# Kernel tuning notes

Hardware: AMD Instinct MI355X
Metric: run time of the kernel (lower is better)

The kernel has to match this reference:

```python
import jax, jax.numpy as jnp
import numpy as np

B, S, D, H, L = 2, 2048, 768, 12, 12
DH = D // H
REL_POS_BINS, MAX_REL_POS = 32, 128
REL_2D_POS_BINS, MAX_REL_2D_POS = 64, 256
LN_EPS = 1e-12


def setup_inputs() -> dict:
    key = jax.random.key(0)
    ks = jax.random.split(key, 12)
    s = 0.02
    return {
        "hidden_states": jax.random.normal(ks[0], (B, S, D), jnp.float32),
        "attention_mask": jnp.zeros((B, 1, 1, S), jnp.bool_),  # True = masked
        "position_ids": jnp.sort(jax.random.randint(ks[1], (B, S), 0, 1024), axis=-1),
        "bbox": jax.random.randint(ks[2], (B, S, 4), 0, 1024),
        # stacked per-layer params (torch Linear applied as x @ W + b)
        "q_w": jax.random.normal(ks[3], (L, D, D), jnp.float32) * s,
        "q_b": jnp.zeros((L, D), jnp.float32),
        "k_w": jax.random.normal(ks[4], (L, D, D), jnp.float32) * s,
        "k_b": jnp.zeros((L, D), jnp.float32),
        "v_w": jax.random.normal(ks[5], (L, D, D), jnp.float32) * s,
        "v_b": jnp.zeros((L, D), jnp.float32),
        "o_w": jax.random.normal(ks[6], (L, D, D), jnp.float32) * s,
        "o_b": jnp.zeros((L, D), jnp.float32),
        "ln_g": jnp.ones((L, D), jnp.float32),
        "ln_b": jnp.zeros((L, D), jnp.float32),
        # rel-pos bias heads x buckets (nn.Linear(bins, heads, bias=False).weight)
        "rel_pos_bias_w": jax.random.normal(ks[7], (H, REL_POS_BINS), jnp.float32) * s,
        "rel_x_bias_w": jax.random.normal(ks[8], (H, REL_2D_POS_BINS), jnp.float32) * s,
        "rel_y_bias_w": jax.random.normal(ks[9], (H, REL_2D_POS_BINS), jnp.float32) * s,
    }


def _rel_bucket(rel, num_buckets, max_distance):
    # bidirectional bucketing from Mesh-TF / ErnieLayout
    nb = num_buckets // 2
    ret = (rel > 0).astype(jnp.int32) * nb
    n = jnp.abs(rel).astype(jnp.int32)
    max_exact = nb // 2
    is_small = n < max_exact
    nf = jnp.maximum(n, 1).astype(jnp.float32)  # avoid log(0); masked by is_small
    val_large = max_exact + (
        jnp.log(nf / max_exact) / np.log(max_distance / max_exact) * (nb - max_exact)
    ).astype(jnp.int32)
    val_large = jnp.minimum(val_large, nb - 1)
    return ret + jnp.where(is_small, n, val_large)


def _bias_from_table(ids_1d, table, num_buckets, max_distance):
    # ids_1d: [B,S] int; table: [H, buckets] -> bias [B,H,S,S]
    rel = ids_1d[:, None, :] - ids_1d[:, :, None]  # memory - query
    buckets = _rel_bucket(rel, num_buckets, max_distance)  # [B,S,S]
    return jnp.transpose(table.T[buckets], (0, 3, 1, 2))  # one-hot @ W.T == gather


def _layer_norm(x, g, b):
    m = jnp.mean(x, axis=-1, keepdims=True)
    v = jnp.mean((x - m) ** 2, axis=-1, keepdims=True)
    return (x - m) / jnp.sqrt(v + LN_EPS) * g + b


def reference(hidden_states, attention_mask, position_ids, bbox,
              q_w, q_b, k_w, k_b, v_w, v_b, o_w, o_b, ln_g, ln_b,
              rel_pos_bias_w, rel_x_bias_w, rel_y_bias_w):
    rel_pos = _bias_from_table(position_ids, rel_pos_bias_w, REL_POS_BINS, MAX_REL_POS)
    rel_2d = (_bias_from_table(bbox[:, :, 0], rel_x_bias_w, REL_2D_POS_BINS, MAX_REL_2D_POS)
              + _bias_from_table(bbox[:, :, 3], rel_y_bias_w, REL_2D_POS_BINS, MAX_REL_2D_POS))
    bias = rel_pos + rel_2d  # [B,H,S,S], shared across layers
    neg = jnp.finfo(jnp.float32).min
    inv_sqrt_dh = 1.0 / np.sqrt(DH)

    def layer(h, p):
        qw, qb, kw, kb, vw, vb, ow, ob, g, bb = p
        q = (h @ qw + qb).reshape(B, S, H, DH).transpose(0, 2, 1, 3) * inv_sqrt_dh
        k = (h @ kw + kb).reshape(B, S, H, DH).transpose(0, 2, 1, 3)
        v = (h @ vw + vb).reshape(B, S, H, DH).transpose(0, 2, 1, 3)
        scores = jnp.einsum('bhqd,bhkd->bhqk', q, k) + bias
        scores = jnp.where(attention_mask, neg, scores)
        probs = jax.nn.softmax(scores, axis=-1)
        ctx = jnp.einsum('bhqk,bhkd->bhqd', probs, v).transpose(0, 2, 1, 3).reshape(B, S, D)
        out = ctx @ ow + ob  # ErnieLayoutSelfOutput dense
        return _layer_norm(out + h, g, bb), None

    h, _ = jax.lax.scan(layer, hidden_states,
                        (q_w, q_b, k_w, k_b, v_w, v_b, o_w, o_b, ln_g, ln_b))
    return h
```

## Files before the change

### kernel.cpp

```cpp
#include <hip/hip_runtime.h>


#define BB 2
#define SS 2048
#define DD 768
#define HH 12
#define NLAYER 12
#define MM 4096

typedef unsigned short u16;
typedef __attribute__((ext_vector_type(8))) short bf16x8;
typedef __attribute__((ext_vector_type(4))) float f32x4;

#define LOG2E 1.44269504088896340736f

__device__ __forceinline__ u16 f2bf(float f) {
  unsigned u = __float_as_uint(f);
  unsigned r = (u + 0x7FFFu + ((u >> 16) & 1u)) >> 16;
  return (u16)r;
}
__device__ __forceinline__ float bf2f(unsigned u) {
  return __uint_as_float(u << 16);
}
__device__ __forceinline__ unsigned cvtpk(float a, float b) {
  unsigned r;
  asm("v_cvt_pk_bf16_f32 %0, %1, %2" : "=v"(r) : "v"(a), "v"(b));
  return r;
}
__device__ __forceinline__ float exp2v(float x) {
  float r;
  asm("v_exp_f32 %0, %1" : "=v"(r) : "v"(x));
  return r;
}

__device__ __forceinline__ void g2lds16(const void* g, void* l) {
  __builtin_amdgcn_global_load_lds(
      (const __attribute__((address_space(1))) unsigned int*)g,
      (__attribute__((address_space(3))) unsigned int*)l, 16, 0, 0);
}

__global__ __launch_bounds__(256) void k_hb(const float4* __restrict__ x,
                                            uint2* __restrict__ o, int n4) {
  int i = blockIdx.x * 256 + threadIdx.x;
  if (i < n4) {
    float4 v = x[i];
    uint2 r;
    r.x = (unsigned)f2bf(v.x) | ((unsigned)f2bf(v.y) << 16);
    r.y = (unsigned)f2bf(v.z) | ((unsigned)f2bf(v.w) << 16);
    o[i] = r;
  }
}

__device__ __forceinline__ int bucket1(int rel) {
  int ret = rel > 0 ? 16 : 0;
  int n = rel < 0 ? -rel : rel;
  if (n < 8) return ret + n;
  int v = 8 + (int)(logf((float)n * 0.125f) * 2.8853900817779268f);
  return ret + (v < 15 ? v : 15);
}
__device__ __forceinline__ int bucket2(int rel) {
  int ret = rel > 0 ? 32 : 0;
  int n = rel < 0 ? -rel : rel;
  if (n < 16) return ret + n;
  int v = 16 + (int)(logf((float)n * 0.0625f) * 5.7707801635558537f);
  return ret + (v < 31 ? v : 31);
}

__global__ __launch_bounds__(256) void k_bias(
    const int* __restrict__ pos, const int* __restrict__ bbx,
    const unsigned char* __restrict__ msk,
    const float* __restrict__ wp, const float* __restrict__ wx,
    const float* __restrict__ wy, u16* __restrict__ bias) {
  int bid = blockIdx.x;
  int g = bid >> 11, rem = bid & 2047;
  int b = rem >> 10, qt = (rem >> 5) & 31, kt = rem & 31;
  __shared__ __align__(16) float swpT[32][4], swxT[64][4], swyT[64][4];
  __shared__ int pq[64], xq[64], yq[64], pk[64], xk[64], yk[64];
  __shared__ unsigned char mk[64];
  int t = threadIdx.x;
  if (t < 128) swpT[t >> 2][t & 3] = wp[(g * 4 + (t & 3)) * 32 + (t >> 2)];
  { int i = t; swxT[i >> 2][i & 3] = wx[(g * 4 + (i & 3)) * 64 + (i >> 2)];
    swyT[i >> 2][i & 3] = wy[(g * 4 + (i & 3)) * 64 + (i >> 2)]; }
  int q0 = qt * 64, k0 = kt * 64;
  if (t < 64) {
    int gi = b * SS + q0 + t;
    pq[t] = pos[gi]; xq[t] = bbx[gi * 4]; yq[t] = bbx[gi * 4 + 3];
  } else if (t < 128) {
    int j = t - 64, gi = b * SS + k0 + j;
    pk[j] = pos[gi]; xk[j] = bbx[gi * 4]; yk[j] = bbx[gi * 4 + 3];
    mk[j] = msk[b * SS + k0 + j];
  }
  __syncthreads();
  int w = t >> 6, l = t & 63;
  int hi = l >> 4;
  int qlr = w * 16 + (l & 15);
  int pql = pq[qlr], xql = xq[qlr], yql = yq[qlr];
  int packed[16];
#pragma unroll
  for (int fn = 0; fn < 4; fn++)
#pragma unroll
    for (int r = 0; r < 4; r++) {
      int kl = fn * 16 + hi * 4 + r;
      int b1 = bucket1(pk[kl] - pql);
      int b2 = bucket2(xk[kl] - xql);
      int b3 = bucket2(yk[kl] - yql);
      packed[fn * 4 + r] = b1 | (b2 << 5) | (b3 << 11) | (mk[kl] ? (1 << 17) : 0);
    }
  unsigned pk2[4][8];
#pragma unroll
  for (int j2 = 0; j2 < 8; j2++) {
    float a0[4], a1[4];
    {
      int p = packed[2 * j2];
      f32x4 ap = *(const f32x4*)swpT[p & 31];
      f32x4 bx = *(const f32x4*)swxT[(p >> 5) & 63];
      f32x4 cy = *(const f32x4*)swyT[(p >> 11) & 63];
      bool mm = (p >> 17) != 0;
#pragma unroll
      for (int hh = 0; hh < 4; hh++)
        a0[hh] = mm ? -3.0e38f : (ap[hh] + bx[hh] + cy[hh]) * LOG2E;
    }
    {
      int p = packed[2 * j2 + 1];
      f32x4 ap = *(const f32x4*)swpT[p & 31];
      f32x4 bx = *(const f32x4*)swxT[(p >> 5) & 63];
      f32x4 cy = *(const f32x4*)swyT[(p >> 11) & 63];
      bool mm = (p >> 17) != 0;
#pragma unroll
      for (int hh = 0; hh < 4; hh++)
        a1[hh] = mm ? -3.0e38f : (ap[hh] + bx[hh] + cy[hh]) * LOG2E;
    }
#pragma unroll
    for (int hh = 0; hh < 4; hh++) pk2[hh][j2] = cvtpk(a0[hh], a1[hh]);
  }
#pragma unroll
  for (int hh = 0; hh < 4; hh++) {
    int h = g * 4 + hh;
    u16* dst = bias +
        ((size_t)((b * 12 + h) * 1024 + qt * 32 + kt) * 256 + t) * 16;
    ((uint4*)dst)[0] = make_uint4(pk2[hh][0], pk2[hh][1], pk2[hh][2], pk2[hh][3]);
    ((uint4*)dst)[1] = make_uint4(pk2[hh][4], pk2[hh][5], pk2[hh][6], pk2[hh][7]);
  }
}

__global__ __launch_bounds__(256) void k_wconv(
    const float* __restrict__ qw, const float* __restrict__ kw,
    const float* __restrict__ vw, const float* __restrict__ ow, int layer,
    u16* __restrict__ wt) {
  int bid = blockIdx.x;
  int g = bid / 144, rr_ = bid % 144, nt = rr_ / 12, kt = rr_ % 12;
  const float* src = g == 0 ? qw : g == 1 ? kw : g == 2 ? vw : ow;
  src += (size_t)layer * DD * DD;
  __shared__ float sm[64][67];
  int t = threadIdx.x, c2 = t & 31, r0 = t >> 5;
#pragma unroll
  for (int p = 0; p < 8; p++) {
    int row = r0 + p * 8;
    float2 v = *(const float2*)&src[(size_t)(kt * 64 + row) * DD + nt * 64 + c2 * 2];
    sm[row][c2 * 2] = v.x;
    sm[row][c2 * 2 + 1] = v.y;
  }
  __syncthreads();
  u16* dst = wt + (size_t)g * DD * DD;
#pragma unroll
  for (int p = 0; p < 8; p++) {
    int n = r0 + p * 8;
    float v0 = sm[c2 * 2][n], v1 = sm[c2 * 2 + 1][n];
    *(unsigned*)&dst[(size_t)(nt * 64 + n) * DD + kt * 64 + c2 * 2] = cvtpk(v0, v1);
  }
}

__device__ __forceinline__ void gemm_core(const u16* __restrict__ A,
                                          const u16* __restrict__ Bt, u16* As,
                                          u16* Bs, f32x4 acc[4][4], int tid) {
  int w = tid >> 6, l = tid & 63;
  int wm = w >> 1, wn = w & 1;
#pragma unroll
  for (int i = 0; i < 4; i++)
#pragma unroll
    for (int j = 0; j < 4; j++) acc[i][j] = f32x4{0.f, 0.f, 0.f, 0.f};
  for (int kt = 0; kt < 12; kt++) {
    __syncthreads();
    int r0 = w * 32;
#pragma unroll
    for (int j = 0; j < 4; j++) {
      int row = r0 + j * 8 + (l >> 3);
      int sl = (l & 7) ^ (row & 7);
      g2lds16(A + (size_t)row * DD + kt * 64 + sl * 8, As + (r0 + j * 8) * 64);
      g2lds16(Bt + (size_t)row * DD + kt * 64 + sl * 8, Bs + (r0 + j * 8) * 64);
    }
    __syncthreads();
#pragma unroll
    for (int kk = 0; kk < 2; kk++) {
      bf16x8 af[4], bfr[4];
#pragma unroll
      for (int fm = 0; fm < 4; fm++) {
        int row = wm * 64 + fm * 16 + (l & 15);
        int slot = (kk * 4 + (l >> 4)) ^ (row & 7);
        af[fm] = *(const bf16x8*)((const char*)As + row * 128 + slot * 16);
      }
#pragma unroll
      for (int fn = 0; fn < 4; fn++) {
        int row = wn * 64 + fn * 16 + (l & 15);
        int slot = (kk * 4 + (l >> 4)) ^ (row & 7);
        bfr[fn] = *(const bf16x8*)((const char*)Bs + row * 128 + slot * 16);
      }
#pragma unroll
      for (int fm = 0; fm < 4; fm++)
#pragma unroll
        for (int fn = 0; fn < 4; fn++)
          acc[fm][fn] = __builtin_amdgcn_mfma_f32_16x16x32_bf16(
              af[fm], bfr[fn], acc[fm][fn], 0, 0, 0);
    }
  }
}

__global__ __launch_bounds__(256) void k_gemm_qkv(
    const u16* __restrict__ hb, const u16* __restrict__ wt,
    const float* __restrict__ qbias, const float* __restrict__ kbias,
    const float* __restrict__ vbias, u16* __restrict__ qo, u16* __restrict__ ko,
    u16* __restrict__ vo) {
  __shared__ __align__(16) u16 As[128 * 64];
  __shared__ __align__(16) u16 Bs[128 * 64];
  int bid = blockIdx.x;
  int mblk = bid / 18, nblk = bid % 18;
  int g = nblk / 6, nb = nblk % 6;
  const u16* A = hb + (size_t)mblk * 128 * DD;
  const u16* Bt = wt + (size_t)g * DD * DD + (size_t)nb * 128 * DD;
  f32x4 acc[4][4];
  gemm_core(A, Bt, As, Bs, acc, threadIdx.x);
  const float* bias = g == 0 ? qbias : g == 1 ? kbias : vbias;
  u16* out = g == 0 ? qo : g == 1 ? ko : vo;
  float scale = g == 0 ? 0.125f * LOG2E : 1.0f;
  int w = threadIdx.x >> 6, l = threadIdx.x & 63;
  int wm = w >> 1, wn = w & 1;
#pragma unroll
  for (int fn = 0; fn < 4; fn++) {
    int col = nb * 128 + wn * 64 + fn * 16 + (l & 15);
    float bval = bias[col];
#pragma unroll
    for (int fm = 0; fm < 4; fm++)
#pragma unroll
      for (int r = 0; r < 4; r++) {
        int row = mblk * 128 + wm * 64 + fm * 16 + ((l >> 4) << 2) + r;
        out[(size_t)row * DD + col] = f2bf((acc[fm][fn][r] + bval) * scale);
      }
  }
}

__global__ __launch_bounds__(256) void k_gemm_o(const u16* __restrict__ ctx,
                                                const u16* __restrict__ wto,
                                                const float* __restrict__ obias,
                                                float* __restrict__ outp) {
  __shared__ __align__(16) u16 As[128 * 64];
  __shared__ __align__(16) u16 Bs[128 * 64];
  int bid = blockIdx.x;
  int mblk = bid / 6, nblk = bid % 6;
  const u16* A = ctx + (size_t)mblk * 128 * DD;
  const u16* Bt = wto + (size_t)nblk * 128 * DD;
  f32x4 acc[4][4];
  gemm_core(A, Bt, As, Bs, acc, threadIdx.x);
  int w = threadIdx.x >> 6, l = threadIdx.x & 63;
  int wm = w >> 1, wn = w & 1;
#pragma unroll
  for (int fn = 0; fn < 4; fn++) {
    int col = nblk * 128 + wn * 64 + fn * 16 + (l & 15);
    float bval = obias[col];
#pragma unroll
    for (int fm = 0; fm < 4; fm++)
#pragma unroll
      for (int r = 0; r < 4; r++) {
        int row = mblk * 128 + wm * 64 + fm * 16 + ((l >> 4) << 2) + r;
        outp[(size_t)row * DD + col] = acc[fm][fn][r] + bval;
      }
  }
}

__global__ __launch_bounds__(256) void k_vt(const u16* __restrict__ vo,
                                            u16* __restrict__ vt) {
  int bid = blockIdx.x;
  int bh = bid >> 5, st = bid & 31;
  int b = bh / 12, h = bh % 12;
  int s0 = st * 64;
  __shared__ u16 sm[64][68];
  int t = threadIdx.x, c = t & 63, r0 = t >> 6;
#pragma unroll
  for (int p = 0; p < 16; p++) {
    int r = r0 + p * 4;
    sm[r][c] = vo[(size_t)(b * SS + s0 + r) * DD + h * 64 + c];
  }
  __syncthreads();
#pragma unroll
  for (int p = 0; p < 16; p++) {
    int d = r0 + p * 4;
    vt[(size_t)(bh * 64 + d) * SS + s0 + c] = sm[c][d];
  }
}

__global__ __launch_bounds__(256) void k_attn(
    const u16* __restrict__ qm, const u16* __restrict__ kmat,
    const u16* __restrict__ vt, const u16* __restrict__ bias,
    u16* __restrict__ ctx) {
  int bid = blockIdx.x;
  int qt = bid & 31, bh = bid >> 5;
  int b = bh / 12, h = bh % 12;
  __shared__ __align__(16) u16 Ks[2][64 * 64];
  __shared__ __align__(16) u16 Vs[2][64 * 64];
  __shared__ __align__(16) u16 Ps[4][16 * 64];
  int tid = threadIdx.x, w = tid >> 6, l = tid & 63;
  int hi = l >> 4, qr = l & 15;
  int q0 = qt * 64;
  const u16* qp = qm + (size_t)(b * SS + q0 + w * 16 + qr) * DD + h * 64 +
                  hi * 8;
  bf16x8 aq0 = *(const bf16x8*)qp;
  bf16x8 aq1 = *(const bf16x8*)(qp + 32);
  const u16* kb_ = kmat + (size_t)(b * SS) * DD + h * 64;
  const u16* vb_ = vt + (size_t)bh * 64 * SS;
  const u16* bb_ = bias + ((size_t)(bh * 32 + qt) * 32 * 256 + tid) * 16;
  f32x4 oa[4];
#pragma unroll
  for (int fn = 0; fn < 4; fn++) oa[fn] = f32x4{0.f, 0.f, 0.f, 0.f};
  f32x4 lacc = f32x4{0.f, 0.f, 0.f, 0.f};
  float m_ = -3.0e38f;
  bf16x8 vones;
#pragma unroll
  for (int i = 0; i < 8; i++) vones[i] = (short)0x3F80;
  int srow = tid >> 3, sc8 = tid & 7;

  auto STAGE = [&](int kt, int buf) {
#pragma unroll
    for (int j = 0; j < 2; j++) {
      int rr = srow + j * 32;
      int sl = sc8 ^ (rr & 7);
      g2lds16(kb_ + (size_t)(kt * 64 + rr) * DD + sl * 8,
              &Ks[buf][tid * 8 + j * 2048]);
      g2lds16(vb_ + (size_t)rr * SS + kt * 64 + sl * 8,
              &Vs[buf][tid * 8 + j * 2048]);
    }
  };

  STAGE(0, 0);
  uint4 bu0 = ((const uint4*)bb_)[0];
  uint4 bu1 = ((const uint4*)bb_)[1];
  uint4 nb0 = bu0, nb1 = bu1;
  char* pw = (char*)&Ps[w][0] + qr * 128;
  int qs = (qr & 7) << 4;
  __syncthreads();

  for (int kt = 0; kt < 32; kt++) {
    int buf = kt & 1;
    if (kt < 31) {
      STAGE(kt + 1, buf ^ 1);
      const uint4* bpn = (const uint4*)(bb_ + (size_t)(kt + 1) * 4096);
      nb0 = bpn[0];
      nb1 = bpn[1];
    }
    unsigned ua[8] = {bu0.x, bu0.y, bu0.z, bu0.w, bu1.x, bu1.y, bu1.z, bu1.w};
    f32x4 sc[4];
#pragma unroll
    for (int fn = 0; fn < 4; fn++)
#pragma unroll
      for (int r = 0; r < 4; r++) {
        int i = fn * 4 + r;
        unsigned uv = ua[i >> 1];
        sc[fn][r] = bf2f((i & 1) ? (uv >> 16) : (uv & 0xffffu));
      }
#pragma unroll
    for (int kk = 0; kk < 2; kk++) {
      bf16x8 aq = kk == 0 ? aq0 : aq1;
#pragma unroll
      for (int fn = 0; fn < 4; fn++) {
        int row = fn * 16 + qr;
        int slot = (kk * 4 + hi) ^ (row & 7);
        bf16x8 bk = *(const bf16x8*)((const char*)&Ks[buf][0] + row * 128 +
                                     slot * 16);
        sc[fn] = __builtin_amdgcn_mfma_f32_16x16x32_bf16(bk, aq, sc[fn],
                                                         0, 0, 0);
      }
    }
    float pm = fmaxf(fmaxf(fmaxf(sc[0][0], sc[0][1]), fmaxf(sc[0][2], sc[0][3])),
                     fmaxf(fmaxf(sc[1][0], sc[1][1]), fmaxf(sc[1][2], sc[1][3])));
    pm = fmaxf(pm,
         fmaxf(fmaxf(fmaxf(sc[2][0], sc[2][1]), fmaxf(sc[2][2], sc[2][3])),
               fmaxf(fmaxf(sc[3][0], sc[3][1]), fmaxf(sc[3][2], sc[3][3]))));
    pm = fmaxf(pm, __shfl_xor(pm, 16));
    pm = fmaxf(pm, __shfl_xor(pm, 32));
    if (__any(pm > m_ + 8.f)) {
      float mn = fmaxf(m_, pm);
      float f = exp2v(m_ - mn);
#pragma unroll
      for (int fn = 0; fn < 4; fn++)
#pragma unroll
        for (int r = 0; r < 4; r++) oa[fn][r] *= f;
#pragma unroll
      for (int r = 0; r < 4; r++) lacc[r] *= f;
      m_ = mn;
    }
#pragma unroll
    for (int fn = 0; fn < 4; fn++)
#pragma unroll
      for (int r = 0; r < 4; r++) sc[fn][r] = exp2v(sc[fn][r] - m_);
#pragma unroll
    for (int fn = 0; fn < 4; fn++) {
      unsigned w0 = cvtpk(sc[fn][0], sc[fn][1]);
      unsigned w1 = cvtpk(sc[fn][2], sc[fn][3]);
      *(uint2*)(pw + ((fn * 32 + hi * 8) ^ qs)) = make_uint2(w0, w1);
    }
#pragma unroll
    for (int ck = 0; ck < 2; ck++) {
      bf16x8 pt = *(const bf16x8*)(pw + ((ck * 64 + hi * 16) ^ qs));
#pragma unroll
      for (int fn = 0; fn < 4; fn++) {
        int row = fn * 16 + qr;
        int slot = (ck * 4 + hi) ^ (row & 7);
        bf16x8 av = *(const bf16x8*)((const char*)&Vs[buf][0] + row * 128 +
                                     slot * 16);
        oa[fn] = __builtin_amdgcn_mfma_f32_16x16x32_bf16(av, pt, oa[fn],
                                                         0, 0, 0);
      }
      lacc = __builtin_amdgcn_mfma_f32_16x16x32_bf16(vones, pt, lacc, 0, 0, 0);
    }
    bu0 = nb0;
    bu1 = nb1;
    __syncthreads();
  }
  float inv = 1.0f / lacc[0];
  u16* cp = ctx + (size_t)(b * SS + q0 + w * 16 + qr) * DD + h * 64 + hi * 4;
#pragma unroll
  for (int fn = 0; fn < 4; fn++) {
    unsigned w0 = cvtpk(oa[fn][0] * inv, oa[fn][1] * inv);
    unsigned w1 = cvtpk(oa[fn][2] * inv, oa[fn][3] * inv);
    *(uint2*)(cp + fn * 16) = make_uint2(w0, w1);
  }
}

__global__ __launch_bounds__(256) void k_ln(const float* __restrict__ x,
                                            const float* __restrict__ res,
                                            const float* __restrict__ g,
                                            const float* __restrict__ bta,
                                            float* __restrict__ ho,
                                            u16* __restrict__ hbo) {
  int w = threadIdx.x >> 6, l = threadIdx.x & 63;
  int row = blockIdx.x * 4 + w;
  const float* xr = x + (size_t)row * DD;
  const float* rr = res + (size_t)row * DD;
  float v[12];
  float s = 0.f, s2 = 0.f;
#pragma unroll
  for (int j = 0; j < 12; j++) {
    float a = xr[l + j * 64] + rr[l + j * 64];
    v[j] = a;
    s += a;
    s2 += a * a;
  }
#pragma unroll
  for (int m = 1; m < 64; m <<= 1) {
    s += __shfl_xor(s, m);
    s2 += __shfl_xor(s2, m);
  }
  float mean = s * (1.f / 768.f);
  float var = s2 * (1.f / 768.f) - mean * mean;
  float rstd = rsqrtf(var + 1e-12f);
#pragma unroll
  for (int j = 0; j < 12; j++) {
    int c = l + j * 64;
    float y = (v[j] - mean) * rstd * g[c] + bta[c];
    ho[(size_t)row * DD + c] = y;
    hbo[(size_t)row * DD + c] = f2bf(y);
  }
}

extern "C" void kernel_launch(void* const* d_in, const int* in_sizes, int n_in,
                              void* d_out, int out_size, void* d_ws,
                              size_t ws_size, hipStream_t stream) {
  const float* hid = (const float*)d_in[0];
  const unsigned char* msk = (const unsigned char*)d_in[1];
  const int* pos = (const int*)d_in[2];
  const int* bbx = (const int*)d_in[3];
  const float* qw = (const float*)d_in[4];
  const float* qbv = (const float*)d_in[5];
  const float* kw = (const float*)d_in[6];
  const float* kbv = (const float*)d_in[7];
  const float* vw = (const float*)d_in[8];
  const float* vbv = (const float*)d_in[9];
  const float* ow = (const float*)d_in[10];
  const float* obv = (const float*)d_in[11];
  const float* lng = (const float*)d_in[12];
  const float* lnb = (const float*)d_in[13];
  const float* wpb = (const float*)d_in[14];
  const float* wxb = (const float*)d_in[15];
  const float* wyb = (const float*)d_in[16];
  float* outp = (float*)d_out;

  char* p = (char*)d_ws;
  u16* bias = (u16*)p;   p += (size_t)201326592;
  float* hbuf = (float*)p; p += 12582912;
  u16* hb = (u16*)p;     p += 6291456;
  u16* qo = (u16*)p;     p += 6291456;
  u16* ko = (u16*)p;     p += 6291456;
  u16* vo = (u16*)p;     p += 6291456;
  u16* vtb = (u16*)p;    p += 6291456;
  u16* ctxb = (u16*)p;   p += 6291456;
  u16* wtb = (u16*)p;    p += 4718592;
  float* att = (float*)qo;

  k_hb<<<dim3(3072), dim3(256), 0, stream>>>((const float4*)hid, (uint2*)hb,
                                             786432);
  k_bias<<<dim3(6144), dim3(256), 0, stream>>>(pos, bbx, msk, wpb, wxb, wyb,
                                               bias);
  for (int l = 0; l < NLAYER; l++) {
    k_wconv<<<dim3(576), dim3(256), 0, stream>>>(qw, kw, vw, ow, l, wtb);
    k_gemm_qkv<<<dim3(576), dim3(256), 0, stream>>>(
        hb, wtb, qbv + l * DD, kbv + l * DD, vbv + l * DD, qo, ko, vo);
    k_vt<<<dim3(768), dim3(256), 0, stream>>>(vo, vtb);
    k_attn<<<dim3(768), dim3(256), 0, stream>>>(qo, ko, vtb, bias, ctxb);
    k_gemm_o<<<dim3(192), dim3(256), 0, stream>>>(
        ctxb, wtb + (size_t)3 * DD * DD, obv + l * DD, att);
    k_ln<<<dim3(1024), dim3(256), 0, stream>>>(
        att, l == 0 ? hid : (const float*)hbuf, lng + l * DD, lnb + l * DD,
        l == 11 ? outp : hbuf, hb);
  }
}
```

Before: 1.647 ms.

## Store attention bias in FP8 and compute all head groups per bias block

```diff
diff --git a/kernel.cpp b/kernel.cpp
--- a/kernel.cpp
+++ b/kernel.cpp
@@ -9,8 +9,10 @@
 #define MM 4096
 
 typedef unsigned short u16;
+typedef unsigned char u8;
 typedef __attribute__((ext_vector_type(8))) short bf16x8;
 typedef __attribute__((ext_vector_type(4))) float f32x4;
+typedef __attribute__((ext_vector_type(2))) float f32x2;
 
 #define LOG2E 1.44269504088896340736f
 
@@ -18,9 +20,6 @@
   unsigned u = __float_as_uint(f);
   unsigned r = (u + 0x7FFFu + ((u >> 16) & 1u)) >> 16;
   return (u16)r;
-}
-__device__ __forceinline__ float bf2f(unsigned u) {
-  return __uint_as_float(u << 16);
 }
 __device__ __forceinline__ unsigned cvtpk(float a, float b) {
   unsigned r;
@@ -70,17 +69,22 @@
     const int* __restrict__ pos, const int* __restrict__ bbx,
     const unsigned char* __restrict__ msk,
     const float* __restrict__ wp, const float* __restrict__ wx,
-    const float* __restrict__ wy, u16* __restrict__ bias) {
+    const float* __restrict__ wy, u8* __restrict__ bias) {
   int bid = blockIdx.x;
-  int g = bid >> 11, rem = bid & 2047;
-  int b = rem >> 10, qt = (rem >> 5) & 31, kt = rem & 31;
-  __shared__ __align__(16) float swpT[32][4], swxT[64][4], swyT[64][4];
+  int b = bid >> 10, qt = (bid >> 5) & 31, kt = bid & 31;
+  __shared__ __align__(16) float swpT[3][32][4], swxT[3][64][4], swyT[3][64][4];
   __shared__ int pq[64], xq[64], yq[64], pk[64], xk[64], yk[64];
   __shared__ unsigned char mk[64];
   int t = threadIdx.x;
-  if (t < 128) swpT[t >> 2][t & 3] = wp[(g * 4 + (t & 3)) * 32 + (t >> 2)];
-  { int i = t; swxT[i >> 2][i & 3] = wx[(g * 4 + (i & 3)) * 64 + (i >> 2)];
-    swyT[i >> 2][i & 3] = wy[(g * 4 + (i & 3)) * 64 + (i >> 2)]; }
+  for (int i = t; i < 384; i += 256) {
+    int g = i >> 7, idx = i & 127;
+    swpT[g][idx >> 2][idx & 3] = wp[(g * 4 + (idx & 3)) * 32 + (idx >> 2)] * LOG2E;
+  }
+  for (int i = t; i < 768; i += 256) {
+    int g = i >> 8, idx = i & 255;
+    swxT[g][idx >> 2][idx & 3] = wx[(g * 4 + (idx & 3)) * 64 + (idx >> 2)] * LOG2E;
+    swyT[g][idx >> 2][idx & 3] = wy[(g * 4 + (idx & 3)) * 64 + (idx >> 2)] * LOG2E;
+  }
   int q0 = qt * 64, k0 = kt * 64;
   if (t < 64) {
     int gi = b * SS + q0 + t;
@@ -106,40 +110,51 @@
       int b3 = bucket2(yk[kl] - yql);
       packed[fn * 4 + r] = b1 | (b2 << 5) | (b3 << 11) | (mk[kl] ? (1 << 17) : 0);
     }
-  unsigned pk2[4][8];
-#pragma unroll
-  for (int j2 = 0; j2 < 8; j2++) {
-    float a0[4], a1[4];
-    {
-      int p = packed[2 * j2];
-      f32x4 ap = *(const f32x4*)swpT[p & 31];
-      f32x4 bx = *(const f32x4*)swxT[(p >> 5) & 63];
-      f32x4 cy = *(const f32x4*)swyT[(p >> 11) & 63];
-      bool mm = (p >> 17) != 0;
-#pragma unroll
-      for (int hh = 0; hh < 4; hh++)
-        a0[hh] = mm ? -3.0e38f : (ap[hh] + bx[hh] + cy[hh]) * LOG2E;
-    }
-    {
-      int p = packed[2 * j2 + 1];
-      f32x4 ap = *(const f32x4*)swpT[p & 31];
-      f32x4 bx = *(const f32x4*)swxT[(p >> 5) & 63];
-      f32x4 cy = *(const f32x4*)swyT[(p >> 11) & 63];
-      bool mm = (p >> 17) != 0;
-#pragma unroll
-      for (int hh = 0; hh < 4; hh++)
-        a1[hh] = mm ? -3.0e38f : (ap[hh] + bx[hh] + cy[hh]) * LOG2E;
-    }
-#pragma unroll
-    for (int hh = 0; hh < 4; hh++) pk2[hh][j2] = cvtpk(a0[hh], a1[hh]);
-  }
-#pragma unroll
-  for (int hh = 0; hh < 4; hh++) {
-    int h = g * 4 + hh;
-    u16* dst = bias +
-        ((size_t)((b * 12 + h) * 1024 + qt * 32 + kt) * 256 + t) * 16;
-    ((uint4*)dst)[0] = make_uint4(pk2[hh][0], pk2[hh][1], pk2[hh][2], pk2[hh][3]);
-    ((uint4*)dst)[1] = make_uint4(pk2[hh][4], pk2[hh][5], pk2[hh][6], pk2[hh][7]);
+  for (int hg = 0; hg < 3; hg++) {
+    unsigned words[4][4];
+#pragma unroll
+    for (int j2 = 0; j2 < 8; j2++) {
+      float a0[4], a1[4];
+      {
+        int p = packed[2 * j2];
+        f32x4 ap = *(const f32x4*)swpT[hg][p & 31];
+        f32x4 bx = *(const f32x4*)swxT[hg][(p >> 5) & 63];
+        f32x4 cy = *(const f32x4*)swyT[hg][(p >> 11) & 63];
+        bool mm = (p >> 17) != 0;
+#pragma unroll
+        for (int hh = 0; hh < 4; hh++)
+          a0[hh] = mm ? -3.0e38f : (ap[hh] + bx[hh] + cy[hh]);
+      }
+      {
+        int p = packed[2 * j2 + 1];
+        f32x4 ap = *(const f32x4*)swpT[hg][p & 31];
+        f32x4 bx = *(const f32x4*)swxT[hg][(p >> 5) & 63];
+        f32x4 cy = *(const f32x4*)swyT[hg][(p >> 11) & 63];
+        bool mm = (p >> 17) != 0;
+#pragma unroll
+        for (int hh = 0; hh < 4; hh++)
+          a1[hh] = mm ? -3.0e38f : (ap[hh] + bx[hh] + cy[hh]);
+      }
+      int wd = j2 >> 1;
+      if ((j2 & 1) == 0) {
+#pragma unroll
+        for (int hh = 0; hh < 4; hh++)
+          words[hh][wd] = __builtin_amdgcn_cvt_pk_fp8_f32(a0[hh], a1[hh], 0, false);
+      } else {
+#pragma unroll
+        for (int hh = 0; hh < 4; hh++)
+          words[hh][wd] = __builtin_amdgcn_cvt_pk_fp8_f32(a0[hh], a1[hh],
+                                                          words[hh][wd], true);
+      }
+    }
+#pragma unroll
+    for (int hh = 0; hh < 4; hh++) {
+      int h = hg * 4 + hh;
+      u8* dst = bias +
+          ((size_t)((b * 12 + h) * 1024 + qt * 32 + kt) * 256 + t) * 16;
+      *(uint4*)dst = make_uint4(words[hh][0], words[hh][1], words[hh][2],
+                                words[hh][3]);
+    }
   }
 }
 
@@ -299,7 +314,7 @@
 
 __global__ __launch_bounds__(256) void k_attn(
     const u16* __restrict__ qm, const u16* __restrict__ kmat,
-    const u16* __restrict__ vt, const u16* __restrict__ bias,
+    const u16* __restrict__ vt, const u8* __restrict__ bias,
     u16* __restrict__ ctx) {
   int bid = blockIdx.x;
   int qt = bid & 31, bh = bid >> 5;
@@ -316,7 +331,7 @@
   bf16x8 aq1 = *(const bf16x8*)(qp + 32);
   const u16* kb_ = kmat + (size_t)(b * SS) * DD + h * 64;
   const u16* vb_ = vt + (size_t)bh * 64 * SS;
-  const u16* bb_ = bias + ((size_t)(bh * 32 + qt) * 32 * 256 + tid) * 16;
+  const u8* bb_ = bias + ((size_t)(bh * 32 + qt) * 32 * 256 + tid) * 16;
   f32x4 oa[4];
 #pragma unroll
   for (int fn = 0; fn < 4; fn++) oa[fn] = f32x4{0.f, 0.f, 0.f, 0.f};
@@ -340,9 +355,8 @@
   };
 
   STAGE(0, 0);
-  uint4 bu0 = ((const uint4*)bb_)[0];
-  uint4 bu1 = ((const uint4*)bb_)[1];
-  uint4 nb0 = bu0, nb1 = bu1;
+  uint4 bu = *(const uint4*)bb_;
+  uint4 nb = bu;
   char* pw = (char*)&Ps[w][0] + qr * 128;
   int qs = (qr & 7) << 4;
   __syncthreads();
@@ -351,20 +365,19 @@
     int buf = kt & 1;
     if (kt < 31) {
       STAGE(kt + 1, buf ^ 1);
-      const uint4* bpn = (const uint4*)(bb_ + (size_t)(kt + 1) * 4096);
-      nb0 = bpn[0];
-      nb1 = bpn[1];
-    }
-    unsigned ua[8] = {bu0.x, bu0.y, bu0.z, bu0.w, bu1.x, bu1.y, bu1.z, bu1.w};
+      nb = *(const uint4*)(bb_ + (size_t)(kt + 1) * 4096);
+    }
     f32x4 sc[4];
-#pragma unroll
-    for (int fn = 0; fn < 4; fn++)
-#pragma unroll
-      for (int r = 0; r < 4; r++) {
-        int i = fn * 4 + r;
-        unsigned uv = ua[i >> 1];
-        sc[fn][r] = bf2f((i & 1) ? (uv >> 16) : (uv & 0xffffu));
-      }
+    {
+      unsigned uw[4] = {bu.x, bu.y, bu.z, bu.w};
+#pragma unroll
+      for (int fn = 0; fn < 4; fn++) {
+        f32x2 p0 = __builtin_amdgcn_cvt_pk_f32_fp8(uw[fn], false);
+        f32x2 p1 = __builtin_amdgcn_cvt_pk_f32_fp8(uw[fn], true);
+        sc[fn][0] = p0.x; sc[fn][1] = p0.y; sc[fn][2] = p1.x; sc[fn][3] = p1.y;
+      }
+    }
+    __builtin_amdgcn_s_setprio(1);
 #pragma unroll
     for (int kk = 0; kk < 2; kk++) {
       bf16x8 aq = kk == 0 ? aq0 : aq1;
@@ -378,6 +391,7 @@
                                                          0, 0, 0);
       }
     }
+    __builtin_amdgcn_s_setprio(0);
     float pm = fmaxf(fmaxf(fmaxf(sc[0][0], sc[0][1]), fmaxf(sc[0][2], sc[0][3])),
                      fmaxf(fmaxf(sc[1][0], sc[1][1]), fmaxf(sc[1][2], sc[1][3])));
     pm = fmaxf(pm,
@@ -406,6 +420,7 @@
       unsigned w1 = cvtpk(sc[fn][2], sc[fn][3]);
       *(uint2*)(pw + ((fn * 32 + hi * 8) ^ qs)) = make_uint2(w0, w1);
     }
+    __builtin_amdgcn_s_setprio(1);
 #pragma unroll
     for (int ck = 0; ck < 2; ck++) {
       bf16x8 pt = *(const bf16x8*)(pw + ((ck * 64 + hi * 16) ^ qs));
@@ -420,8 +435,8 @@
       }
       lacc = __builtin_amdgcn_mfma_f32_16x16x32_bf16(vones, pt, lacc, 0, 0, 0);
     }
-    bu0 = nb0;
-    bu1 = nb1;
+    __builtin_amdgcn_s_setprio(0);
+    bu = nb;
     __syncthreads();
   }
   float inv = 1.0f / lacc[0];
@@ -493,7 +508,7 @@
   float* outp = (float*)d_out;
 
   char* p = (char*)d_ws;
-  u16* bias = (u16*)p;   p += (size_t)201326592;
+  u8* bias = (u8*)p;     p += (size_t)100663296;
   float* hbuf = (float*)p; p += 12582912;
   u16* hb = (u16*)p;     p += 6291456;
   u16* qo = (u16*)p;     p += 6291456;
@@ -506,7 +521,7 @@
 
   k_hb<<<dim3(3072), dim3(256), 0, stream>>>((const float4*)hid, (uint2*)hb,
                                              786432);
-  k_bias<<<dim3(6144), dim3(256), 0, stream>>>(pos, bbx, msk, wpb, wxb, wyb,
+  k_bias<<<dim3(2048), dim3(256), 0, stream>>>(pos, bbx, msk, wpb, wxb, wyb,
                                                bias);
   for (int l = 0; l < NLAYER; l++) {
     k_wconv<<<dim3(576), dim3(256), 0, stream>>>(qw, kw, vw, ow, l, wtb);
```

New measurement: 1.532 ms. 1.07x faster.
